# Performance work log

Hardware: AMD Instinct MI355X
Metric: run time of the kernel (lower is better)

Reference implementation:

```python
import jax, jax.numpy as jnp
import numpy as np

NUM_STEPS = 151            # num_steps from __init__
STEP = 2.0 / (NUM_STEPS - 1)
HALF = (NUM_STEPS - 1) // 2  # bin offset: t_j = -1 + j*STEP, 1/STEP = HALF
N = 4096
D = 512
NUM_CLASSES = 751


def _soft_histogram(s, mask, size):
    # Triangular-kernel (linear) soft binning, equivalent to the original
    # indsa/indsb masked-repeat construction: each similarity s in
    # [t_{j-1}, t_j] contributes (1-frac) to bin j-1 and frac to bin j.
    x = s / STEP
    k = jnp.floor(x)           # zero-gradient, plays the role of s_repeat_floor
    frac = x - k               # (s - (t_j - STEP)) / STEP
    kI = k.astype(jnp.int32)
    idx_lo = jnp.clip(kI + HALF, 0, NUM_STEPS - 1)
    idx_hi = jnp.clip(kI + HALF + 1, 0, NUM_STEPS - 1)
    hist = jnp.zeros((NUM_STEPS,), dtype=s.dtype)
    hist = hist.at[idx_lo].add((1.0 - frac) * mask)
    hist = hist.at[idx_hi].add(frac * mask)
    return hist / size


def setup_inputs() -> dict:
    key = jax.random.key(0)
    kf, kc = jax.random.split(key)
    return {
        "features": jax.random.normal(kf, (N, D), dtype=jnp.float32),
        "classes": jax.random.randint(kc, (N,), 0, NUM_CLASSES, dtype=jnp.int32),
    }


def reference(features, classes):
    # L2Normalization
    f = features / jnp.linalg.norm(features, axis=1, keepdims=True)
    dists = f @ f.T                                   # [N, N] cosine sims
    iu, ju = np.triu_indices(features.shape[0], 1)    # static upper-tri pairs
    s = dists[iu, ju]                                 # [P] P = N(N-1)/2
    pos = (classes[iu] == classes[ju]).astype(s.dtype)
    neg = 1.0 - pos
    hist_pos = _soft_histogram(s, pos, jnp.sum(pos))
    hist_neg = _soft_histogram(s, neg, jnp.sum(neg))
    cdf_pos = jnp.cumsum(hist_pos)                    # tril-masked column sums == cumsum
    return jnp.sum(hist_neg * cdf_pos)
```

## Files before the change

### kernel.cpp

```cpp
#include <hip/hip_runtime.h>
#include <math.h>

#define N 4096
#define D 512
#define NUM_STEPS 151
#define HALF_BINS 75
#define INV_STEP 75.0f
#define NUM_CLASSES 751
#define P_TOTAL 8386560.0f
#define GTILES 64
#define NTILES (GTILES * (GTILES + 1) / 2)

#define WS_SUM_ALL 0
#define WS_POS_CNT 1
#define WS_SUM_POS 2
#define WS_S_POS   3
#define WS_G_OFF   8
#define WS_BSUM_OFF 256
#define WS_LIST_OFF 4096
#define MAXP (1 << 18)
#define WS_PAIR_OFF (WS_LIST_OFF + MAXP)
#define WS_FEAT_OFF (WS_PAIR_OFF + 2 * MAXP)
#define WS_FEATB_OFF (WS_FEAT_OFF + N * D)

typedef __bf16 bf16x8 __attribute__((ext_vector_type(8)));
typedef float floatx4 __attribute__((ext_vector_type(4)));

__device__ __forceinline__ void load_lds16(const void* g, void* s) {
    __builtin_amdgcn_global_load_lds(
        (const __attribute__((address_space(1))) void*)g,
        (__attribute__((address_space(3))) void*)s, 16, 0, 0);
}

__global__ __launch_bounds__(256) void k_prep(const float* __restrict__ feat,
                                              const int* __restrict__ cls,
                                              float* __restrict__ nf,
                                              __bf16* __restrict__ nfb,
                                              int2* __restrict__ pairRows,
                                              int* __restrict__ posCntOut,
                                              float* __restrict__ sPosOut) {
    __shared__ int shmem[NUM_CLASSES * 3 + N / 4];
    __shared__ int wsumR[4], wsumP[4];
    __shared__ float wsumF[4];
    int t = threadIdx.x;

    if (blockIdx.x < N) {
        int row = blockIdx.x;
        const float* fr = feat + (size_t)row * D;
        float a = fr[t];
        float b = fr[t + 256];
        float ss = a * a + b * b;
        for (int o = 32; o > 0; o >>= 1) ss += __shfl_down(ss, o, 64);
        int lane = t & 63, wid = t >> 6;
        if (lane == 0) wsumF[wid] = ss;
        __syncthreads();
        float tot = wsumF[0] + wsumF[1] + wsumF[2] + wsumF[3];
        float inv = 1.0f / sqrtf(tot);
        float na = a * inv, nb = b * inv;
        nf[(size_t)row * D + t] = na;
        nf[(size_t)row * D + t + 256] = nb;
        nfb[(size_t)row * D + t] = (__bf16)na;
        nfb[(size_t)row * D + t + 256] = (__bf16)nb;
        return;
    }

    int* hcnt = shmem;
    int* hoff = shmem + NUM_CLASSES;
    int* poff = shmem + 2 * NUM_CLASSES;
    __shared__ int rowIdxL[N / 2];
    for (int c = t; c < NUM_CLASSES; c += 256) hcnt[c] = 0;
    __syncthreads();
    for (int n = t; n < N; n += 256) atomicAdd(&hcnt[cls[n]], 1);
    __syncthreads();

    int c0 = t * 3;
    int cntPreR[3], cntPreP[3];
    int myR = 0, myP = 0;
    #pragma unroll
    for (int k = 0; k < 3; ++k) {
        int c = c0 + k;
        int cnt = (c < NUM_CLASSES) ? hcnt[c] : 0;
        cntPreR[k] = myR; cntPreP[k] = myP;
        myR += cnt;
        myP += cnt * (cnt - 1) / 2;
    }
    int lane = t & 63, wv = t >> 6;
    int incR = myR, incP = myP;
    for (int o = 1; o < 64; o <<= 1) {
        int rr = __shfl_up(incR, o, 64);
        int pp = __shfl_up(incP, o, 64);
        if (lane >= o) { incR += rr; incP += pp; }
    }
    if (lane == 63) { wsumR[wv] = incR; wsumP[wv] = incP; }
    __syncthreads();
    int baseR = 0, baseP = 0;
    for (int w = 0; w < wv; ++w) { baseR += wsumR[w]; baseP += wsumP[w]; }
    int exR = baseR + incR - myR;
    int exP = baseP + incP - myP;
    #pragma unroll
    for (int k = 0; k < 3; ++k) {
        int c = c0 + k;
        if (c < NUM_CLASSES) { hoff[c] = exR + cntPreR[k]; poff[c] = exP + cntPreP[k]; }
    }
    __syncthreads();

    for (int c = t; c < NUM_CLASSES; c += 256) hcnt[c] = hoff[c];
    __syncthreads();
    for (int n = t; n < N; n += 256) {
        int p = atomicAdd(&hcnt[cls[n]], 1);
        int word = p >> 1, sh = (p & 1) * 16;
        atomicAnd(&rowIdxL[word], ~(0xFFFF << sh));
        atomicOr(&rowIdxL[word], (n & 0xFFFF) << sh);
    }
    __syncthreads();

    for (int c = t; c < NUM_CLASSES; c += 256) {
        int o0 = hoff[c];
        int nc = (c + 1 < NUM_CLASSES ? hoff[c + 1]
                                      : wsumR[0] + wsumR[1] + wsumR[2] + wsumR[3]) - o0;
        int pb = poff[c];
        int idx = 0;
        for (int a = 0; a < nc - 1; ++a) {
            int sa = o0 + a;
            int ra = (rowIdxL[sa >> 1] >> ((sa & 1) * 16)) & 0xFFFF;
            for (int b = a + 1; b < nc; ++b) {
                int sb = o0 + b;
                int rb = (rowIdxL[sb >> 1] >> ((sb & 1) * 16)) & 0xFFFF;
                pairRows[pb + idx] = make_int2(ra, rb);
                ++idx;
            }
        }
    }
    if (t == 0) {
        int totP = wsumP[0] + wsumP[1] + wsumP[2] + wsumP[3];
        *posCntOut = totP;
        *sPosOut = (float)totP;
    }
}

__global__ __launch_bounds__(256) void k_pospairs4(const float* __restrict__ nf,
                                                   const int2* __restrict__ pairRows,
                                                   const int* __restrict__ posCnt,
                                                   float* __restrict__ posS) {
    int nP = *posCnt;
    if (nP > MAXP) nP = MAXP;
    int gw = (blockIdx.x * 256 + threadIdx.x) >> 6;
    int lane = threadIdx.x & 63;
    for (int p = gw; p < nP; p += 4096) {
        int2 pr = pairRows[p];
        const float4* x4 = (const float4*)(nf + (size_t)pr.x * D);
        const float4* y4 = (const float4*)(nf + (size_t)pr.y * D);
        float4 xa = x4[lane * 2], xb = x4[lane * 2 + 1];
        float4 ya = y4[lane * 2], yb = y4[lane * 2 + 1];
        float s = xa.x * ya.x + xa.y * ya.y + xa.z * ya.z + xa.w * ya.w
                + xb.x * yb.x + xb.y * yb.y + xb.z * yb.z + xb.w * yb.w;
        for (int o = 32; o > 0; o >>= 1) s += __shfl_down(s, o, 64);
        if (lane == 0) posS[p] = s;
    }
}

__global__ __launch_bounds__(256) void k_build_cdf(const float* __restrict__ posS,
                                                   const int* __restrict__ posCnt,
                                                   float* __restrict__ G,
                                                   float* __restrict__ sumPosOut) {
    __shared__ float hist[NUM_STEPS];
    __shared__ float Gs[NUM_STEPS];
    int t = threadIdx.x;
    int C = *posCnt;
    if (C > MAXP) C = MAXP;
    for (int b = t; b < NUM_STEPS; b += 256) hist[b] = 0.f;
    __syncthreads();
    for (int p = t; p < C; p += 256) {
        float s = posS[p];
        float x = s * INV_STEP;
        float kf = floorf(x);
        float frac = x - kf;
        int kI = (int)kf;
        int lo = min(max(kI + HALF_BINS, 0), NUM_STEPS - 1);
        int hi = min(max(kI + HALF_BINS + 1, 0), NUM_STEPS - 1);
        atomicAdd(&hist[lo], 1.0f - frac);
        atomicAdd(&hist[hi], frac);
    }
    __syncthreads();
    if (t == 0) {
        float invC = (C > 0) ? (1.0f / (float)C) : 0.f;
        float acc = 0.f;
        for (int b = 0; b < NUM_STEPS; ++b) {
            acc += hist[b];
            Gs[b] = acc * invC;
        }
    }
    __syncthreads();
    for (int b = t; b < NUM_STEPS; b += 256) G[b] = Gs[b];
    float ps = 0.f;
    for (int p = t; p < C; p += 256) {
        float s = posS[p];
        float x = s * INV_STEP;
        float kf = floorf(x);
        float frac = x - kf;
        int kI = (int)kf;
        int lo = min(max(kI + HALF_BINS, 0), NUM_STEPS - 1);
        int hi = min(max(kI + HALF_BINS + 1, 0), NUM_STEPS - 1);
        ps += (1.f - frac) * Gs[lo] + frac * Gs[hi];
    }
    for (int o = 32; o > 0; o >>= 1) ps += __shfl_down(ps, o, 64);
    __shared__ float wsum[4];
    int lane = t & 63, wid = t >> 6;
    if (lane == 0) wsum[wid] = ps;
    __syncthreads();
    if (t == 0) *sumPosOut = wsum[0] + wsum[1] + wsum[2] + wsum[3];
}

__global__ __launch_bounds__(256) void k_gram(const __bf16* __restrict__ nfb,
                                              const float* __restrict__ G,
                                              float* __restrict__ blockSums) {
    int bid = blockIdx.x;
    int ti = 0, rem = bid;
    while (rem >= GTILES - ti) { rem -= GTILES - ti; ++ti; }
    int tj = ti + rem;

    __shared__ __align__(16) __bf16 As[4 * 512];
    __shared__ __align__(16) __bf16 Bs[4 * 512];
    __shared__ float Gs[NUM_STEPS];

    int tid = threadIdx.x;
    for (int b = tid; b < NUM_STEPS; b += 256) Gs[b] = G[b];

    int lane = tid & 63;
    int wave = tid >> 6;
    int rh = wave >> 1, ch = wave & 1;
    int rowA0 = ti * 64, rowB0 = tj * 64;

    int fr2 = lane & 15, kc2 = lane >> 4;
    const __bf16* gA = nfb + (size_t)(rowA0 + wave * 16 + fr2) * D + kc2 * 8;
    const __bf16* gB = nfb + (size_t)(rowB0 + wave * 16 + fr2) * D + kc2 * 8;
    __bf16* lA = &As[wave * 512];
    __bf16* lB = &Bs[wave * 512];

    floatx4 acc[2][2] = {};

    for (int kb = 0; kb < D / 32; ++kb) {
        int kbase = kb * 32;
        load_lds16(gA + kbase, lA);
        load_lds16(gB + kbase, lB);
        __syncthreads();

        bf16x8 a[2], b[2];
        #pragma unroll
        for (int r = 0; r < 2; ++r)
            a[r] = *(const bf16x8*)(&As[(rh * 2 + r) * 512 + lane * 8]);
        #pragma unroll
        for (int c = 0; c < 2; ++c)
            b[c] = *(const bf16x8*)(&Bs[(ch * 2 + c) * 512 + lane * 8]);
        #pragma unroll
        for (int r = 0; r < 2; ++r)
            #pragma unroll
            for (int c = 0; c < 2; ++c)
                acc[r][c] = __builtin_amdgcn_mfma_f32_16x16x32_bf16(a[r], b[c], acc[r][c], 0, 0, 0);
        __syncthreads();
    }

    int crow = (lane >> 4) * 4;
    int ccol = lane & 15;
    float gsum = 0.f;
    #pragma unroll
    for (int r = 0; r < 2; ++r) {
        #pragma unroll
        for (int c = 0; c < 2; ++c) {
            #pragma unroll
            for (int reg = 0; reg < 4; ++reg) {
                int gi = rowA0 + rh * 32 + r * 16 + crow + reg;
                int gj = rowB0 + ch * 32 + c * 16 + ccol;
                if (gi < gj) {
                    float s = acc[r][c][reg];
                    float x = s * INV_STEP;
                    float kf = floorf(x);
                    float frac = x - kf;
                    int kI = (int)kf;
                    int lo = min(max(kI + HALF_BINS, 0), NUM_STEPS - 1);
                    int hi = min(max(kI + HALF_BINS + 1, 0), NUM_STEPS - 1);
                    gsum += (1.f - frac) * Gs[lo] + frac * Gs[hi];
                }
            }
        }
    }
    for (int o = 32; o > 0; o >>= 1) gsum += __shfl_down(gsum, o, 64);
    __shared__ float wsum[4];
    if ((tid & 63) == 0) wsum[tid >> 6] = gsum;
    __syncthreads();
    if (tid == 0) blockSums[bid] = wsum[0] + wsum[1] + wsum[2] + wsum[3];
}

__global__ __launch_bounds__(256) void k_final(const float* __restrict__ blockSums,
                                               const float* __restrict__ wsf,
                                               float* __restrict__ out) {
    int t = threadIdx.x;
    float s = 0.f;
    for (int i = t; i < NTILES; i += 256) s += blockSums[i];
    for (int o = 32; o > 0; o >>= 1) s += __shfl_down(s, o, 64);
    __shared__ float wsum[4];
    if ((t & 63) == 0) wsum[t >> 6] = s;
    __syncthreads();
    if (t == 0) {
        float sAll = wsum[0] + wsum[1] + wsum[2] + wsum[3];
        float sPos = wsf[WS_SUM_POS];
        float C = wsf[WS_S_POS];
        out[0] = (sAll - sPos) / (P_TOTAL - C);
    }
}

extern "C" void kernel_launch(void* const* d_in, const int* in_sizes, int n_in,
                              void* d_out, int out_size, void* d_ws, size_t ws_size,
                              hipStream_t stream) {
    const float* feat = (const float*)d_in[0];
    const int* cls = (const int*)d_in[1];
    float* out = (float*)d_out;
    float* wsf = (float*)d_ws;
    int* wsi = (int*)d_ws;

    hipMemsetAsync(d_ws, 0, 1024, stream);

    float* nf = wsf + WS_FEAT_OFF;
    __bf16* nfb = (__bf16*)(wsf + WS_FEATB_OFF);
    float* posS = wsf + WS_LIST_OFF;
    int2* pairRows = (int2*)(wsi + WS_PAIR_OFF);
    float* G = wsf + WS_G_OFF;
    float* blockSums = wsf + WS_BSUM_OFF;

    k_prep<<<N + 1, 256, 0, stream>>>(feat, cls, nf, nfb, pairRows,
                                      wsi + WS_POS_CNT, wsf + WS_S_POS);
    k_pospairs4<<<1024, 256, 0, stream>>>(nf, pairRows, wsi + WS_POS_CNT, posS);
    k_build_cdf<<<1, 256, 0, stream>>>(posS, wsi + WS_POS_CNT, G, wsf + WS_SUM_POS);
    k_gram<<<NTILES, 256, 0, stream>>>(nfb, G, blockSums);
    k_final<<<1, 256, 0, stream>>>(blockSums, wsf, out);
}
```

Measured before the change: 172.8 us.

## Enlarge gram tiles to 128x128 with double-buffered register-prefetched LDS

Doubles the gram tile edge to 128 rows with 8 waves per block, each computing a 32x64 subtile, so each loaded operand is reused across more MFMAs. Replaces direct global-to-LDS loads with register prefetch into a double-buffered LDS, cutting one barrier per k-step and overlapping the next load with the MFMAs. This adds register and LDS pressure and reduces the block count to 528, which may leave CUs less full and waste more of the diagonal tiles.

```diff
diff --git a/kernel.cpp b/kernel.cpp
--- a/kernel.cpp
+++ b/kernel.cpp
@@ -8,8 +8,8 @@
 #define INV_STEP 75.0f
 #define NUM_CLASSES 751
 #define P_TOTAL 8386560.0f
-#define GTILES 64
-#define NTILES (GTILES * (GTILES + 1) / 2)
+#define TILES_1D 32
+#define NTILES (TILES_1D * (TILES_1D + 1) / 2)
 
 #define WS_SUM_ALL 0
 #define WS_POS_CNT 1
@@ -25,12 +25,6 @@
 
 typedef __bf16 bf16x8 __attribute__((ext_vector_type(8)));
 typedef float floatx4 __attribute__((ext_vector_type(4)));
-
-__device__ __forceinline__ void load_lds16(const void* g, void* s) {
-    __builtin_amdgcn_global_load_lds(
-        (const __attribute__((address_space(1))) void*)g,
-        (__attribute__((address_space(3))) void*)s, 16, 0, 0);
-}
 
 __global__ __launch_bounds__(256) void k_prep(const float* __restrict__ feat,
                                               const int* __restrict__ cls,
@@ -211,53 +205,64 @@
     if (t == 0) *sumPosOut = wsum[0] + wsum[1] + wsum[2] + wsum[3];
 }
 
-__global__ __launch_bounds__(256) void k_gram(const __bf16* __restrict__ nfb,
+__global__ __launch_bounds__(512) void k_gram(const __bf16* __restrict__ nfb,
                                               const float* __restrict__ G,
                                               float* __restrict__ blockSums) {
     int bid = blockIdx.x;
     int ti = 0, rem = bid;
-    while (rem >= GTILES - ti) { rem -= GTILES - ti; ++ti; }
+    while (rem >= TILES_1D - ti) { rem -= TILES_1D - ti; ++ti; }
     int tj = ti + rem;
 
-    __shared__ __align__(16) __bf16 As[4 * 512];
-    __shared__ __align__(16) __bf16 Bs[4 * 512];
+    __shared__ __align__(16) __bf16 As[2][8 * 512];
+    __shared__ __align__(16) __bf16 Bs[2][8 * 512];
     __shared__ float Gs[NUM_STEPS];
 
     int tid = threadIdx.x;
-    for (int b = tid; b < NUM_STEPS; b += 256) Gs[b] = G[b];
+    for (int b = tid; b < NUM_STEPS; b += 512) Gs[b] = G[b];
 
     int lane = tid & 63;
     int wave = tid >> 6;
-    int rh = wave >> 1, ch = wave & 1;
-    int rowA0 = ti * 64, rowB0 = tj * 64;
+    int wr = wave >> 1;
+    int wc = wave & 1;
+    int rowA0 = ti * 128, rowB0 = tj * 128;
 
     int fr2 = lane & 15, kc2 = lane >> 4;
     const __bf16* gA = nfb + (size_t)(rowA0 + wave * 16 + fr2) * D + kc2 * 8;
     const __bf16* gB = nfb + (size_t)(rowB0 + wave * 16 + fr2) * D + kc2 * 8;
-    __bf16* lA = &As[wave * 512];
-    __bf16* lB = &Bs[wave * 512];
-
-    floatx4 acc[2][2] = {};
+    int ldsSlot = wave * 512 + lane * 8;
+
+    floatx4 acc[2][4] = {};
+
+    float4 ra = *(const float4*)(gA);
+    float4 rb = *(const float4*)(gB);
+    *(float4*)(&As[0][ldsSlot]) = ra;
+    *(float4*)(&Bs[0][ldsSlot]) = rb;
 
     for (int kb = 0; kb < D / 32; ++kb) {
-        int kbase = kb * 32;
-        load_lds16(gA + kbase, lA);
-        load_lds16(gB + kbase, lB);
         __syncthreads();
-
-        bf16x8 a[2], b[2];
+        int cur = kb & 1;
+        if (kb < D / 32 - 1) {
+            ra = *(const float4*)(gA + (kb + 1) * 32);
+            rb = *(const float4*)(gB + (kb + 1) * 32);
+        }
+
+        bf16x8 a[2], b[4];
         #pragma unroll
         for (int r = 0; r < 2; ++r)
-            a[r] = *(const bf16x8*)(&As[(rh * 2 + r) * 512 + lane * 8]);
-        #pragma unroll
-        for (int c = 0; c < 2; ++c)
-            b[c] = *(const bf16x8*)(&Bs[(ch * 2 + c) * 512 + lane * 8]);
+            a[r] = *(const bf16x8*)(&As[cur][(wr * 2 + r) * 512 + lane * 8]);
+        #pragma unroll
+        for (int c = 0; c < 4; ++c)
+            b[c] = *(const bf16x8*)(&Bs[cur][(wc * 4 + c) * 512 + lane * 8]);
         #pragma unroll
         for (int r = 0; r < 2; ++r)
             #pragma unroll
-            for (int c = 0; c < 2; ++c)
+            for (int c = 0; c < 4; ++c)
                 acc[r][c] = __builtin_amdgcn_mfma_f32_16x16x32_bf16(a[r], b[c], acc[r][c], 0, 0, 0);
-        __syncthreads();
+
+        if (kb < D / 32 - 1) {
+            *(float4*)(&As[cur ^ 1][ldsSlot]) = ra;
+            *(float4*)(&Bs[cur ^ 1][ldsSlot]) = rb;
+        }
     }
 
     int crow = (lane >> 4) * 4;
@@ -266,11 +271,11 @@
     #pragma unroll
     for (int r = 0; r < 2; ++r) {
         #pragma unroll
-        for (int c = 0; c < 2; ++c) {
+        for (int c = 0; c < 4; ++c) {
             #pragma unroll
             for (int reg = 0; reg < 4; ++reg) {
-                int gi = rowA0 + rh * 32 + r * 16 + crow + reg;
-                int gj = rowB0 + ch * 32 + c * 16 + ccol;
+                int gi = rowA0 + (wr * 2 + r) * 16 + crow + reg;
+                int gj = rowB0 + (wc * 4 + c) * 16 + ccol;
                 if (gi < gj) {
                     float s = acc[r][c][reg];
                     float x = s * INV_STEP;
@@ -285,10 +290,15 @@
         }
     }
     for (int o = 32; o > 0; o >>= 1) gsum += __shfl_down(gsum, o, 64);
-    __shared__ float wsum[4];
+    __shared__ float wsum[8];
     if ((tid & 63) == 0) wsum[tid >> 6] = gsum;
     __syncthreads();
-    if (tid == 0) blockSums[bid] = wsum[0] + wsum[1] + wsum[2] + wsum[3];
+    if (tid == 0) {
+        float s = 0.f;
+        #pragma unroll
+        for (int w = 0; w < 8; ++w) s += wsum[w];
+        blockSums[bid] = s;
+    }
 }
 
 __global__ __launch_bounds__(256) void k_final(const float* __restrict__ blockSums,
@@ -331,6 +341,6 @@
                                       wsi + WS_POS_CNT, wsf + WS_S_POS);
     k_pospairs4<<<1024, 256, 0, stream>>>(nf, pairRows, wsi + WS_POS_CNT, posS);
     k_build_cdf<<<1, 256, 0, stream>>>(posS, wsi + WS_POS_CNT, G, wsf + WS_SUM_POS);
-    k_gram<<<NTILES, 256, 0, stream>>>(nfb, G, blockSums);
+    k_gram<<<NTILES, 512, 0, stream>>>(nfb, G, blockSums);
     k_final<<<1, 256, 0, stream>>>(blockSums, wsf, out);
 }
```

Measured after the change: 162.9 us. 5.7% less time.
